# Performance work log

Measured on AMD Instinct MI355X. Metric: run time of the kernel, lower is better.

## Reference

```python
import jax, jax.numpy as jnp
import numpy as np

B, N, D = 2048, 128, 32   # samples, features, per-feature embed dim
H = 8                     # num_head
ND = N * D                # flattened width = 4096
U = D * N // H            # per-head units = 512
DH = D // H               # per-head output feature dim = 4


def setup_inputs() -> dict:
    key = jax.random.key(0)
    k_x, k_q, k_k, k_v, k_o = jax.random.split(key, 5)
    scale_w = 0.02  # keep QK^T logits in a sane range for softmax
    x = jax.random.normal(k_x, (B, N, D), dtype=jnp.float32)
    Wq = jax.random.normal(k_q, (H, ND, U), dtype=jnp.float32) * scale_w
    Wk = jax.random.normal(k_k, (H, ND, U), dtype=jnp.float32) * scale_w
    Wv = jax.random.normal(k_v, (H, ND, U), dtype=jnp.float32) * scale_w
    Wo = jax.random.normal(k_o, (D, D), dtype=jnp.float32) * (1.0 / np.sqrt(D))
    return {"x": x, "Wq": Wq, "Wk": Wk, "Wv": Wv, "Wo": Wo}


def reference(x, Wq, Wk, Wv, Wo):
    b, n, d = x.shape
    scale = d ** (-0.5)          # note: original scales by feature dim d, not head dim
    xf = x.reshape(b, n * d)     # (b, nd); the leading 1 axis in TF is vacuous
    # Batched per-head projections (collapses the Python head loop into one GEMM each)
    q = jnp.einsum('bf,hfu->hbu', xf, Wq)   # (H, b, U)
    k = jnp.einsum('bf,hfu->hbu', xf, Wk)   # (H, b, U)
    v = jnp.einsum('bf,hfu->hbu', xf, Wv)   # (H, b, U)
    scores = jax.nn.softmax(jnp.einsum('hbu,hcu->hbc', q, k) * scale, axis=-1)  # (H, b, b)
    av = jnp.einsum('hbc,hcu->hbu', scores, v)              # (H, b, U)
    # per-head reshape (b, U) -> (b, n, d/H), then concat heads along last dim
    av = av.reshape(H, b, n, d // H)                         # (H, b, n, dh)
    concat = jnp.transpose(av, (1, 2, 0, 3)).reshape(b, n, d)  # (b, n, d)
    return concat @ Wo  # dropout rate is 0 -> identity
```

## Files before the change

### kernel.cpp

```cpp
#include <hip/hip_runtime.h>
#include <stdint.h>
#include <math.h>

typedef short    s16x8 __attribute__((ext_vector_type(8)));
typedef float    f32x4 __attribute__((ext_vector_type(4)));
typedef uint32_t u32x4 __attribute__((ext_vector_type(4)));
typedef unsigned short u16x4 __attribute__((ext_vector_type(4)));

__device__ __forceinline__ uint16_t f2bf(float f) {
  union { float f; uint32_t u; } v; v.f = f;
  uint32_t r = v.u + 0x7fffu + ((v.u >> 16) & 1u);
  return (uint16_t)(r >> 16);
}
__device__ __forceinline__ float bf2f(uint16_t h) {
  union { uint32_t u; float f; } v; v.u = ((uint32_t)h) << 16;
  return v.f;
}

__device__ __forceinline__ void gld16(const void* g, void* l) {
  __builtin_amdgcn_global_load_lds(
      (const __attribute__((address_space(1))) void*)g,
      (__attribute__((address_space(3))) void*)l, 16, 0, 0);
}

__global__ __launch_bounds__(256) void cvt_x(const float* __restrict__ x,
                                             uint16_t* __restrict__ xf,
                                             float* __restrict__ rs) {
  if (blockIdx.x < 64) rs[blockIdx.x * 256 + threadIdx.x] = 0.f;
  size_t i = ((size_t)blockIdx.x * 256 + threadIdx.x) * 4;
  f32x4 v = *(const f32x4*)(x + i);
  u16x4 o = { f2bf(v.x), f2bf(v.y), f2bf(v.z), f2bf(v.w) };
  *(u16x4*)(xf + i) = o;
}

__global__ __launch_bounds__(256) void wtrans(const float* __restrict__ W0,
                                              const float* __restrict__ W1,
                                              const float* __restrict__ W2,
                                              uint16_t* __restrict__ Wt) {
  const int z = blockIdx.z;
  const float* W = (z < 8 ? W0 : (z < 16 ? W1 : W2)) + (size_t)(z & 7) * (4096 * 512);
  const int f0 = blockIdx.x * 32, u0 = blockIdx.y * 32;
  __shared__ float t[32][33];
  const int tid = threadIdx.x;
  {
    const int fi = tid >> 3, uu = (tid & 7) * 4;
    f32x4 v = *(const f32x4*)(W + (size_t)(f0 + fi) * 512 + u0 + uu);
    t[fi][uu] = v.x; t[fi][uu + 1] = v.y; t[fi][uu + 2] = v.z; t[fi][uu + 3] = v.w;
  }
  __syncthreads();
  {
    const int ui = tid >> 3, ff = (tid & 7) * 4;
    u16x4 o = { f2bf(t[ff][ui]), f2bf(t[ff + 1][ui]),
                f2bf(t[ff + 2][ui]), f2bf(t[ff + 3][ui]) };
    *(u16x4*)&Wt[((size_t)z * 512 + u0 + ui) * 4096 + f0 + ff] = o;
  }
}

template <int MODE>
__global__ __launch_bounds__(256, 2) void gemm_bt(
    const uint16_t* __restrict__ A, size_t sAz,
    const uint16_t* __restrict__ B, size_t sBz,
    void* __restrict__ C0, void* __restrict__ C1,
    int K, float scale, float* __restrict__ rs) {
  const int tid = threadIdx.x;
  const int wave = tid >> 6, lane = tid & 63;
  const int quad = lane >> 4, l16 = lane & 15;
  const int wrow = (wave >> 1) * 64, wcol = (wave & 1) * 64;
  const int m0 = blockIdx.y * 128, n0 = blockIdx.x * 128;
  const int z = blockIdx.z;
  A += (size_t)z * sAz;
  B += (size_t)z * sBz;

  __shared__ __align__(16) uint16_t lA[128 * 32];
  __shared__ __align__(16) uint16_t lB[128 * 32];

  f32x4 acc[4][4];
#pragma unroll
  for (int i = 0; i < 4; i++)
#pragma unroll
    for (int j = 0; j < 4; j++) acc[i][j] = f32x4{0.f, 0.f, 0.f, 0.f};

  const int r0 = wave * 16 + (lane >> 2);
  const int cg = ((lane & 3) ^ ((lane >> 3) & 3)) * 8;
  const uint16_t* gA = A + (size_t)(m0 + r0) * K + cg;
  const uint16_t* gB = B + (size_t)(n0 + r0) * K + cg;
  const size_t row64 = (size_t)64 * K;
  uint16_t* sA0 = &lA[wave * 512];
  uint16_t* sA1 = &lA[2048 + wave * 512];
  uint16_t* sB0 = &lB[wave * 512];
  uint16_t* sB1 = &lB[2048 + wave * 512];

  const int fsw = (quad ^ ((l16 >> 1) & 3)) * 8;

  for (int k0 = 0; k0 < K; k0 += 32) {
    __syncthreads();
    gld16(gA, sA0);
    gld16(gA + row64, sA1);
    gld16(gB, sB0);
    gld16(gB + row64, sB1);
    gA += 32; gB += 32;
    __syncthreads();
    s16x8 af[4], bfr[4];
#pragma unroll
    for (int i = 0; i < 4; i++)
      af[i] = *(const s16x8*)&lA[(wrow + i * 16 + l16) * 32 + fsw];
#pragma unroll
    for (int j = 0; j < 4; j++)
      bfr[j] = *(const s16x8*)&lB[(wcol + j * 16 + l16) * 32 + fsw];
#pragma unroll
    for (int i = 0; i < 4; i++)
#pragma unroll
      for (int j = 0; j < 4; j++)
        acc[i][j] = __builtin_amdgcn_mfma_f32_16x16x32_bf16(af[i], bfr[j], acc[i][j], 0, 0, 0);
  }

  const int mb = m0 + wrow + quad * 4;
  const int nb = n0 + wcol + l16;
  if (MODE == 4) {
    if (z < 16) {
      uint16_t* C = (uint16_t*)C0 + ((size_t)z << 20);
#pragma unroll
      for (int i = 0; i < 4; i++)
#pragma unroll
        for (int j = 0; j < 4; j++)
#pragma unroll
          for (int r = 0; r < 4; r++)
            C[(size_t)(mb + i * 16 + r) * 512 + (nb + j * 16)] = f2bf(acc[i][j][r]);
    } else {
      uint16_t* C = (uint16_t*)C1 + ((size_t)(z - 16) << 20);
#pragma unroll
      for (int i = 0; i < 4; i++)
#pragma unroll
        for (int j = 0; j < 4; j++) {
          u16x4 o = { f2bf(acc[i][j][0]), f2bf(acc[i][j][1]),
                      f2bf(acc[i][j][2]), f2bf(acc[i][j][3]) };
          *(u16x4*)&((uint16_t*)C)[(size_t)(nb + j * 16) * 2048 + (mb + i * 16)] = o;
        }
    }
  } else if (MODE == 2) {
    uint16_t* C = (uint16_t*)C0 + ((size_t)z << 22);
    float* rz = rs + (z << 11);
    float si[4][4];
#pragma unroll
    for (int i = 0; i < 4; i++)
#pragma unroll
      for (int r = 0; r < 4; r++) si[i][r] = 0.f;
#pragma unroll
    for (int i = 0; i < 4; i++)
#pragma unroll
      for (int j = 0; j < 4; j++)
#pragma unroll
        for (int r = 0; r < 4; r++) {
          float e = exp2f(fmaf(acc[i][j][r], scale, -43.2808512f));
          uint16_t hb = f2bf(e);
          C[(size_t)(mb + i * 16 + r) * 2048 + (nb + j * 16)] = hb;
          si[i][r] += bf2f(hb);
        }
#pragma unroll
    for (int i = 0; i < 4; i++)
#pragma unroll
      for (int r = 0; r < 4; r++) {
        float s = si[i][r];
        s += __shfl_xor(s, 1);
        s += __shfl_xor(s, 2);
        s += __shfl_xor(s, 4);
        s += __shfl_xor(s, 8);
        si[i][r] = s;
      }
    if (l16 == 0) {
#pragma unroll
      for (int i = 0; i < 4; i++)
#pragma unroll
        for (int r = 0; r < 4; r++)
          atomicAdd(&rz[mb + i * 16 + r], si[i][r]);
    }
  } else {
    float* C = (float*)C0 + ((size_t)z << 20);
    const float* rz = rs + (z << 11);
#pragma unroll
    for (int i = 0; i < 4; i++)
#pragma unroll
      for (int r = 0; r < 4; r++) {
        float w = 1.0f / rz[mb + i * 16 + r];
#pragma unroll
        for (int j = 0; j < 4; j++)
          C[(size_t)(mb + i * 16 + r) * 512 + (nb + j * 16)] = acc[i][j][r] * w;
      }
  }
}

__global__ __launch_bounds__(256) void out_proj(const float* __restrict__ av,
                                                const float* __restrict__ Wo,
                                                float* __restrict__ out) {
  __shared__ float lw[1024];
  const int tid = threadIdx.x;
#pragma unroll
  for (int i = 0; i < 4; i++) lw[tid + i * 256] = Wo[tid + i * 256];
  __syncthreads();
  const int p = blockIdx.x * 256 + tid;
  const int b = p >> 7, n = p & 127;
  float c[32];
#pragma unroll
  for (int h = 0; h < 8; h++) {
    f32x4 v = *(const f32x4*)(av + ((size_t)h * 2048 + b) * 512 + n * 4);
    c[h * 4] = v.x; c[h * 4 + 1] = v.y; c[h * 4 + 2] = v.z; c[h * 4 + 3] = v.w;
  }
  float o[32];
#pragma unroll
  for (int d = 0; d < 32; d++) o[d] = 0.f;
#pragma unroll
  for (int j = 0; j < 32; j++) {
    float cj = c[j];
#pragma unroll
    for (int d = 0; d < 32; d++) o[d] = fmaf(cj, lw[j * 32 + d], o[d]);
  }
  float* dst = out + (size_t)p * 32;
#pragma unroll
  for (int i = 0; i < 8; i++) {
    f32x4 v = { o[i * 4], o[i * 4 + 1], o[i * 4 + 2], o[i * 4 + 3] };
    *(f32x4*)(dst + i * 4) = v;
  }
}

extern "C" void kernel_launch(void* const* d_in, const int* in_sizes, int n_in,
                              void* d_out, int out_size, void* d_ws, size_t ws_size,
                              hipStream_t stream) {
  const float* x  = (const float*)d_in[0];
  const float* Wq = (const float*)d_in[1];
  const float* Wk = (const float*)d_in[2];
  const float* Wv = (const float*)d_in[3];
  const float* Wo = (const float*)d_in[4];
  float* out = (float*)d_out;

  uint8_t* ws = (uint8_t*)d_ws;
  uint16_t* Wt = (uint16_t*)(ws);
  uint16_t* P  = (uint16_t*)(ws);
  float*    av = (float*)(ws + 67108864);
  uint16_t* xf = (uint16_t*)(ws + 100663296);
  uint16_t* q  = (uint16_t*)(ws + 117440512);
  uint16_t* vt = (uint16_t*)(ws + 150994944);
  float*    rs = (float*)(ws + 167772160);

  const size_t WtH = (size_t)512 * 4096;
  const float scale2 = 0.17677669529663687f * 1.4426950408889634f;

  cvt_x<<<8192, 256, 0, stream>>>(x, xf, rs);
  wtrans<<<dim3(128, 16, 24), 256, 0, stream>>>(Wq, Wk, Wv, Wt);

  gemm_bt<4><<<dim3(4, 16, 24), 256, 0, stream>>>(
      xf, 0, Wt, WtH, q, vt, 4096, 0.f, nullptr);

  gemm_bt<2><<<dim3(16, 16, 8), 256, 0, stream>>>(
      q, (size_t)2048 * 512, q + (size_t)8 * 2048 * 512, (size_t)2048 * 512,
      P, nullptr, 512, scale2, rs);

  gemm_bt<3><<<dim3(4, 16, 8), 256, 0, stream>>>(
      P, (size_t)2048 * 2048, vt, (size_t)512 * 2048,
      av, nullptr, 2048, 0.f, rs);

  out_proj<<<1024, 256, 0, stream>>>(av, Wo, out);
}
```

Before: 615.8 us.

## Double GEMM K-tile to 64 with new LDS swizzle and raise occupancy hint

Each K-step of the bf16 MFMA GEMM now loads 64 elements instead of 32, using a new 8-way XOR swizzle for the LDS layout. This halves the number of barrier pairs per K loop. The launch bounds hint also rises from 2 to 4 blocks per CU, which pushes the compiler to use fewer registers and may cause spills. LDS per block doubles to 32 KB.

```diff
diff --git a/kernel.cpp b/kernel.cpp
--- a/kernel.cpp
+++ b/kernel.cpp
@@ -57,7 +57,7 @@
 }
 
 template <int MODE>
-__global__ __launch_bounds__(256, 2) void gemm_bt(
+__global__ __launch_bounds__(256, 4) void gemm_bt(
     const uint16_t* __restrict__ A, size_t sAz,
     const uint16_t* __restrict__ B, size_t sBz,
     void* __restrict__ C0, void* __restrict__ C1,
@@ -71,8 +71,8 @@
   A += (size_t)z * sAz;
   B += (size_t)z * sBz;
 
-  __shared__ __align__(16) uint16_t lA[128 * 32];
-  __shared__ __align__(16) uint16_t lB[128 * 32];
+  __shared__ __align__(16) uint16_t lA[128 * 64];
+  __shared__ __align__(16) uint16_t lB[128 * 64];
 
   f32x4 acc[4][4];
 #pragma unroll
@@ -80,38 +80,40 @@
 #pragma unroll
     for (int j = 0; j < 4; j++) acc[i][j] = f32x4{0.f, 0.f, 0.f, 0.f};
 
-  const int r0 = wave * 16 + (lane >> 2);
-  const int cg = ((lane & 3) ^ ((lane >> 3) & 3)) * 8;
-  const uint16_t* gA = A + (size_t)(m0 + r0) * K + cg;
-  const uint16_t* gB = B + (size_t)(n0 + r0) * K + cg;
-  const size_t row64 = (size_t)64 * K;
-  uint16_t* sA0 = &lA[wave * 512];
-  uint16_t* sA1 = &lA[2048 + wave * 512];
-  uint16_t* sB0 = &lB[wave * 512];
-  uint16_t* sB1 = &lB[2048 + wave * 512];
-
-  const int fsw = (quad ^ ((l16 >> 1) & 3)) * 8;
-
-  for (int k0 = 0; k0 < K; k0 += 32) {
+  const int lrow = lane >> 3;
+  const int cs = ((lane & 7) ^ (lrow & 7)) * 8;
+  const int rs0 = wave * 8;
+  const uint16_t* gA = A + (size_t)(m0 + rs0 + lrow) * K + cs;
+  const uint16_t* gB = B + (size_t)(n0 + rs0 + lrow) * K + cs;
+  const size_t row32 = (size_t)32 * K;
+  uint16_t* sA = &lA[rs0 * 64];
+  uint16_t* sB = &lB[rs0 * 64];
+
+  for (int k0 = 0; k0 < K; k0 += 64) {
     __syncthreads();
-    gld16(gA, sA0);
-    gld16(gA + row64, sA1);
-    gld16(gB, sB0);
-    gld16(gB + row64, sB1);
-    gA += 32; gB += 32;
+#pragma unroll
+    for (int g = 0; g < 4; g++) {
+      gld16(gA + g * row32, sA + g * 2048);
+      gld16(gB + g * row32, sB + g * 2048);
+    }
+    gA += 64; gB += 64;
     __syncthreads();
-    s16x8 af[4], bfr[4];
-#pragma unroll
-    for (int i = 0; i < 4; i++)
-      af[i] = *(const s16x8*)&lA[(wrow + i * 16 + l16) * 32 + fsw];
-#pragma unroll
-    for (int j = 0; j < 4; j++)
-      bfr[j] = *(const s16x8*)&lB[(wcol + j * 16 + l16) * 32 + fsw];
-#pragma unroll
-    for (int i = 0; i < 4; i++)
+#pragma unroll
+    for (int h = 0; h < 2; h++) {
+      s16x8 af[4], bfr[4];
+      const int fsw = (((h * 4 + quad) ^ (l16 & 7)) * 8);
+#pragma unroll
+      for (int i = 0; i < 4; i++)
+        af[i] = *(const s16x8*)&lA[(wrow + i * 16 + l16) * 64 + fsw];
 #pragma unroll
       for (int j = 0; j < 4; j++)
-        acc[i][j] = __builtin_amdgcn_mfma_f32_16x16x32_bf16(af[i], bfr[j], acc[i][j], 0, 0, 0);
+        bfr[j] = *(const s16x8*)&lB[(wcol + j * 16 + l16) * 64 + fsw];
+#pragma unroll
+      for (int i = 0; i < 4; i++)
+#pragma unroll
+        for (int j = 0; j < 4; j++)
+          acc[i][j] = __builtin_amdgcn_mfma_f32_16x16x32_bf16(af[i], bfr[j], acc[i][j], 0, 0, 0);
+    }
   }
 
   const int mb = m0 + wrow + quad * 4;
```

Result: faster. 572.1 us (-7.1%).
